# Performance work log

Measured on AMD Instinct MI355X. Metric: run time of the kernel, lower is better.

The kernel has to match this reference:

```python
import jax, jax.numpy as jnp
import numpy as np

B, T, C, H, W = 16, 128, 32, 16, 16
NUM_FEAT = 16
D = C * H * W            # conv1d in-channels (kernel size 1 => linear)
G = NUM_FEAT * H * W     # G3 out-channels


def setup_inputs() -> dict:
    key = jax.random.key(0)
    ks = jax.random.split(key, 8)
    s1 = 1.0 / np.sqrt(D)
    return {
        "input1": jax.random.normal(ks[0], (B, T, C, H, W), jnp.float32),
        "input2": jax.random.normal(ks[1], (B, T, C, H, W), jnp.float32),
        "w1": jax.random.uniform(ks[2], (NUM_FEAT, D), jnp.float32, -s1, s1),
        "b1": jax.random.uniform(ks[3], (NUM_FEAT,), jnp.float32, -s1, s1),
        "w2": jax.random.uniform(ks[4], (NUM_FEAT, D), jnp.float32, -s1, s1),
        "b2": jax.random.uniform(ks[5], (NUM_FEAT,), jnp.float32, -s1, s1),
        "w3": jax.random.uniform(ks[6], (G, D), jnp.float32, -s1, s1),
        "b3": jax.random.uniform(ks[7], (G,), jnp.float32, -s1, s1),
    }


def reference(input1, input2, w1, b1, w2, b2, w3, b3):
    b, t = input1.shape[:2]
    x1 = input1.reshape(b, t, D)  # [B,T,D]
    x2 = input2.reshape(b, t, D)
    # Conv1d(kernel=1) projections (channels-first conv == per-frame linear)
    q = jnp.einsum('btd,fd->btf', x1, w1) + b1          # [B,T,F]
    k = jnp.einsum('bsd,fd->bsf', x2, w2) + b2          # [B,S,F]
    scores = jnp.einsum('btf,bsf->bts', q, k)            # [B,T,T]
    attn = jax.nn.softmax(scores, axis=1)                # softmax over dim=1 (rows)
    v = jnp.einsum('bsd,gd->bsg', x1, w3) + b3           # [B,T,G]
    out = jnp.einsum('bts,bsg->btg', attn, v)            # [B,T,G]
    return out.reshape(b, t, NUM_FEAT, H, W)
```

## Files before the change

### kernel.cpp

```cpp
#include <hip/hip_runtime.h>
#include <cstdint>
#include <cstddef>

#define Bn 16
#define Tn 128
#define Dn 8192
#define Fn 16
#define Gn 4096
#define MT (Bn*Tn)

typedef __attribute__((ext_vector_type(8))) short short8;
typedef __attribute__((ext_vector_type(4))) float f32x4;

__device__ inline short f2bf(float f) {
    union { float f; uint32_t u; } c; c.f = f;
    uint32_t u = c.u;
    uint32_t r = (u + 0x7FFFu + ((u >> 16) & 1u)) >> 16;
    return (short)(r & 0xFFFFu);
}

__device__ inline short8 cvt8(float4 a, float4 b) {
    short8 v;
    v[0] = f2bf(a.x); v[1] = f2bf(a.y); v[2] = f2bf(a.z); v[3] = f2bf(a.w);
    v[4] = f2bf(b.x); v[5] = f2bf(b.y); v[6] = f2bf(b.z); v[7] = f2bf(b.w);
    return v;
}

#define N8_X1 (MT * Dn / 8)
#define N8_W3 ((size_t)Gn * Dn / 8)

__global__ __launch_bounds__(256) void cvt2_kernel(
    const float* __restrict__ x1, const float* __restrict__ w3,
    short* __restrict__ x1b, short* __restrict__ w3b)
{
    const size_t total = N8_X1 + N8_W3;
    size_t i = (size_t)blockIdx.x * 256 + threadIdx.x;
    const size_t stride = (size_t)gridDim.x * 256;
    for (; i < total; i += stride) {
        if (i < N8_X1) {
            const float4* s = ((const float4*)x1) + i * 2;
            ((short8*)x1b)[i] = cvt8(s[0], s[1]);
        } else {
            const size_t j = i - N8_X1;
            const float4* s = ((const float4*)w3) + j * 2;
            ((short8*)w3b)[j] = cvt8(s[0], s[1]);
        }
    }
}

__global__ __launch_bounds__(256) void qk_gemm_kernel(
    const short* __restrict__ x1b, const float* __restrict__ x2,
    const float* __restrict__ w1, const float* __restrict__ w2,
    const float* __restrict__ b1, const float* __restrict__ b2,
    float* __restrict__ q, float* __restrict__ k)
{
    __shared__ float red[4][16][16];
    const int tid = threadIdx.x;
    const int tile = blockIdx.x >> 1;
    const int isK  = blockIdx.x & 1;
    const int m0 = tile * 16;
    const int wave = tid >> 6, lane = tid & 63;
    const int quad = lane >> 4, r = lane & 15;
    const int kbase = wave * (Dn / 4);

    f32x4 acc = {};

    if (!isK) {
        const short* ap = x1b + (size_t)(m0 + r) * Dn + kbase + quad * 8;
        const float* bp = w1 + (size_t)r * Dn + kbase + quad * 8;
        #pragma unroll 4
        for (int it = 0; it < 64; ++it) {
            short8 af = *(const short8*)(ap + it * 32);
            const float4* b4 = (const float4*)(bp + it * 32);
            short8 bf = cvt8(b4[0], b4[1]);
            acc = __builtin_amdgcn_mfma_f32_16x16x32_bf16(af, bf, acc, 0, 0, 0);
        }
    } else {
        const float* apf = x2 + (size_t)(m0 + r) * Dn + kbase + quad * 8;
        const float* bp  = w2 + (size_t)r * Dn + kbase + quad * 8;
        #pragma unroll 4
        for (int it = 0; it < 64; ++it) {
            const float4* a4 = (const float4*)(apf + it * 32);
            short8 af = cvt8(a4[0], a4[1]);
            const float4* b4 = (const float4*)(bp + it * 32);
            short8 bf = cvt8(b4[0], b4[1]);
            acc = __builtin_amdgcn_mfma_f32_16x16x32_bf16(af, bf, acc, 0, 0, 0);
        }
    }

    #pragma unroll
    for (int reg = 0; reg < 4; ++reg)
        red[wave][quad * 4 + reg][r] = acc[reg];
    __syncthreads();

    const int m = tid >> 4, f = tid & 15;
    float s = red[0][m][f] + red[1][m][f] + red[2][m][f] + red[3][m][f];
    s += (isK ? b2 : b1)[f];
    (isK ? k : q)[(m0 + m) * Fn + f] = s;
}

__global__ __launch_bounds__(256) void attn_kernel(
    const float* __restrict__ q, const float* __restrict__ k,
    short* __restrict__ attn16)
{
    __shared__ float qs[Tn * 17];
    const int b = blockIdx.x;
    const int tid = threadIdx.x;
    const int wave = tid >> 6, lane = tid & 63;
    const int s = blockIdx.y * 4 + wave;

    for (int i = tid; i < Tn * Fn; i += 256)
        qs[(i >> 4) * 17 + (i & 15)] = q[b * Tn * Fn + i];
    __syncthreads();

    float kr[16];
    #pragma unroll
    for (int f = 0; f < 16; ++f) kr[f] = k[((size_t)b * Tn + s) * Fn + f];

    const int t0 = lane, t1 = lane + 64;
    float sc0 = 0.f, sc1 = 0.f;
    #pragma unroll
    for (int f = 0; f < 16; ++f) {
        sc0 += qs[t0 * 17 + f] * kr[f];
        sc1 += qs[t1 * 17 + f] * kr[f];
    }
    float m = fmaxf(sc0, sc1);
    #pragma unroll
    for (int off = 32; off > 0; off >>= 1)
        m = fmaxf(m, __shfl_xor(m, off, 64));
    const float e0 = __expf(sc0 - m), e1 = __expf(sc1 - m);
    float ssum = e0 + e1;
    #pragma unroll
    for (int off = 32; off > 0; off >>= 1)
        ssum += __shfl_xor(ssum, off, 64);
    const float inv = 1.f / ssum;

    short* ap = attn16 + (size_t)b * Tn * Tn;
    ap[t0 * Tn + s] = f2bf(e0 * inv);
    ap[t1 * Tn + s] = f2bf(e1 * inv);
}

#define BK 32

__global__ __launch_bounds__(256) void gemm_v_split_kernel(
    const short* __restrict__ A, const short* __restrict__ Bw,
    float* __restrict__ vTf, const int kspan)
{
    __shared__ __attribute__((aligned(16))) short As[128 * BK];
    __shared__ __attribute__((aligned(16))) short Bs[128 * BK];

    const int tid = threadIdx.x;
    const int m0 = blockIdx.y * 128;
    const int n0 = blockIdx.x * 128;
    const int z  = blockIdx.z;
    const int kbase = z * kspan;
    float* outp = vTf + (size_t)z * Gn * MT;
    const int wave = tid >> 6, lane = tid & 63;
    const int wm = (wave >> 1) * 64, wn = (wave & 1) * 64;
    const int quad = lane >> 4, r = lane & 15;

    const int srow = wave * 32 + (lane >> 2);
    const int scol = (lane & 3) * 8;
    const short* gA = A  + (size_t)(m0 + srow) * Dn + kbase + scol;
    const short* gB = Bw + (size_t)(n0 + srow) * Dn + kbase + scol;
    short* lA = &As[srow * BK + scol];
    short* lB = &Bs[srow * BK + scol];

    f32x4 acc[4][4] = {};

    #pragma unroll 1
    for (int k0 = 0; k0 < kspan; k0 += BK) {
        __syncthreads();
        __builtin_amdgcn_global_load_lds(
            (const __attribute__((address_space(1))) void*)(gA + k0),
            (__attribute__((address_space(3))) void*)lA, 16, 0, 0);
        __builtin_amdgcn_global_load_lds(
            (const __attribute__((address_space(1))) void*)(gA + k0 + (size_t)16 * Dn),
            (__attribute__((address_space(3))) void*)(lA + 16 * BK), 16, 0, 0);
        __builtin_amdgcn_global_load_lds(
            (const __attribute__((address_space(1))) void*)(gB + k0),
            (__attribute__((address_space(3))) void*)lB, 16, 0, 0);
        __builtin_amdgcn_global_load_lds(
            (const __attribute__((address_space(1))) void*)(gB + k0 + (size_t)16 * Dn),
            (__attribute__((address_space(3))) void*)(lB + 16 * BK), 16, 0, 0);
        __syncthreads();

        short8 af[4], bf[4];
        #pragma unroll
        for (int i = 0; i < 4; ++i)
            af[i] = *(const short8*)&As[(wm + i * 16 + r) * BK + quad * 8];
        #pragma unroll
        for (int j = 0; j < 4; ++j)
            bf[j] = *(const short8*)&Bs[(wn + j * 16 + r) * BK + quad * 8];

        #pragma unroll
        for (int i = 0; i < 4; ++i)
            #pragma unroll
            for (int j = 0; j < 4; ++j)
                acc[i][j] = __builtin_amdgcn_mfma_f32_16x16x32_bf16(
                    af[i], bf[j], acc[i][j], 0, 0, 0);
    }

    #pragma unroll
    for (int i = 0; i < 4; ++i) {
        #pragma unroll
        for (int reg = 0; reg < 4; ++reg) {
            const int rowg = m0 + wm + i * 16 + quad * 4 + reg;
            #pragma unroll
            for (int j = 0; j < 4; ++j) {
                const int col = n0 + wn + j * 16 + r;
                outp[(size_t)rowg * MT + col] = acc[i][j][reg];
            }
        }
    }
}

__global__ __launch_bounds__(256) void vt_cvt_kernel(
    const float* __restrict__ vTf, const float* __restrict__ bias,
    short* __restrict__ vT, const int nparts)
{
    const size_t N8 = (size_t)Gn * MT / 8;
    size_t i = (size_t)blockIdx.x * 256 + threadIdx.x;
    const size_t stride = (size_t)gridDim.x * 256;
    for (; i < N8; i += stride) {
        const float bv = bias[i >> 8];
        float4 a = {bv, bv, bv, bv}, b = {bv, bv, bv, bv};
        for (int p = 0; p < nparts; ++p) {
            const float4* pp = (const float4*)(vTf + (size_t)p * Gn * MT);
            float4 a1 = pp[i * 2], b1 = pp[i * 2 + 1];
            a.x += a1.x; a.y += a1.y; a.z += a1.z; a.w += a1.w;
            b.x += b1.x; b.y += b1.y; b.z += b1.z; b.w += b1.w;
        }
        ((short8*)vT)[i] = cvt8(a, b);
    }
}

__global__ __launch_bounds__(256) void gemm_v_kernel(
    const short* __restrict__ A, const short* __restrict__ Bw,
    const float* __restrict__ bias, short* __restrict__ vT)
{
    __shared__ __attribute__((aligned(16))) short As[128 * BK];
    __shared__ __attribute__((aligned(16))) short Bs[128 * BK];

    const int tid = threadIdx.x;
    const int m0 = blockIdx.y * 128;
    const int n0 = blockIdx.x * 128;
    const int wave = tid >> 6, lane = tid & 63;
    const int wm = (wave >> 1) * 64, wn = (wave & 1) * 64;
    const int quad = lane >> 4, r = lane & 15;

    const int srow = wave * 32 + (lane >> 2);
    const int scol = (lane & 3) * 8;
    const short* gA = A  + (size_t)(m0 + srow) * Dn + scol;
    const short* gB = Bw + (size_t)(n0 + srow) * Dn + scol;
    short* lA = &As[srow * BK + scol];
    short* lB = &Bs[srow * BK + scol];

    f32x4 acc[4][4] = {};

    #pragma unroll 1
    for (int k0 = 0; k0 < Dn; k0 += BK) {
        __syncthreads();
        __builtin_amdgcn_global_load_lds(
            (const __attribute__((address_space(1))) void*)(gA + k0),
            (__attribute__((address_space(3))) void*)lA, 16, 0, 0);
        __builtin_amdgcn_global_load_lds(
            (const __attribute__((address_space(1))) void*)(gA + k0 + (size_t)16 * Dn),
            (__attribute__((address_space(3))) void*)(lA + 16 * BK), 16, 0, 0);
        __builtin_amdgcn_global_load_lds(
            (const __attribute__((address_space(1))) void*)(gB + k0),
            (__attribute__((address_space(3))) void*)lB, 16, 0, 0);
        __builtin_amdgcn_global_load_lds(
            (const __attribute__((address_space(1))) void*)(gB + k0 + (size_t)16 * Dn),
            (__attribute__((address_space(3))) void*)(lB + 16 * BK), 16, 0, 0);
        __syncthreads();

        short8 af[4], bf[4];
        #pragma unroll
        for (int i = 0; i < 4; ++i)
            af[i] = *(const short8*)&As[(wm + i * 16 + r) * BK + quad * 8];
        #pragma unroll
        for (int j = 0; j < 4; ++j)
            bf[j] = *(const short8*)&Bs[(wn + j * 16 + r) * BK + quad * 8];

        #pragma unroll
        for (int i = 0; i < 4; ++i)
            #pragma unroll
            for (int j = 0; j < 4; ++j)
                acc[i][j] = __builtin_amdgcn_mfma_f32_16x16x32_bf16(
                    af[i], bf[j], acc[i][j], 0, 0, 0);
    }

    #pragma unroll
    for (int i = 0; i < 4; ++i) {
        #pragma unroll
        for (int reg = 0; reg < 4; ++reg) {
            const int rowg = m0 + wm + i * 16 + quad * 4 + reg;
            const float bv = bias[rowg];
            #pragma unroll
            for (int j = 0; j < 4; ++j) {
                const int col = n0 + wn + j * 16 + r;
                vT[(size_t)rowg * MT + col] = f2bf(acc[i][j][reg] + bv);
            }
        }
    }
}

__global__ __launch_bounds__(256) void out_gemm_kernel(
    const short* __restrict__ attn16, const short* __restrict__ vT,
    float* __restrict__ out)
{
    __shared__ __attribute__((aligned(16))) short As[128 * BK];
    __shared__ __attribute__((aligned(16))) short Bs[64 * BK];

    const int tid = threadIdx.x;
    const int b  = blockIdx.y;
    const int n0 = blockIdx.x * 64;
    const int wave = tid >> 6, lane = tid & 63;
    const int wm = (wave >> 1) * 64, wn = (wave & 1) * 32;
    const int quad = lane >> 4, r = lane & 15;

    const int srowA = wave * 32 + (lane >> 2);
    const int srowB = wave * 16 + (lane >> 2);
    const int scol = (lane & 3) * 8;
    const short* gA = attn16 + (size_t)b * Tn * Tn + srowA * Tn + scol;
    const short* gB = vT + (size_t)(n0 + srowB) * MT + b * Tn + scol;
    short* lA = &As[srowA * BK + scol];
    short* lB = &Bs[srowB * BK + scol];

    f32x4 acc[4][2] = {};

    #pragma unroll 1
    for (int k0 = 0; k0 < Tn; k0 += BK) {
        __syncthreads();
        __builtin_amdgcn_global_load_lds(
            (const __attribute__((address_space(1))) void*)(gA + k0),
            (__attribute__((address_space(3))) void*)lA, 16, 0, 0);
        __builtin_amdgcn_global_load_lds(
            (const __attribute__((address_space(1))) void*)(gA + k0 + 16 * Tn),
            (__attribute__((address_space(3))) void*)(lA + 16 * BK), 16, 0, 0);
        __builtin_amdgcn_global_load_lds(
            (const __attribute__((address_space(1))) void*)(gB + k0),
            (__attribute__((address_space(3))) void*)lB, 16, 0, 0);
        __syncthreads();

        short8 af[4], bf[2];
        #pragma unroll
        for (int i = 0; i < 4; ++i)
            af[i] = *(const short8*)&As[(wm + i * 16 + r) * BK + quad * 8];
        #pragma unroll
        for (int j = 0; j < 2; ++j)
            bf[j] = *(const short8*)&Bs[(wn + j * 16 + r) * BK + quad * 8];

        #pragma unroll
        for (int i = 0; i < 4; ++i)
            #pragma unroll
            for (int j = 0; j < 2; ++j)
                acc[i][j] = __builtin_amdgcn_mfma_f32_16x16x32_bf16(
                    af[i], bf[j], acc[i][j], 0, 0, 0);
    }

    #pragma unroll
    for (int j = 0; j < 2; ++j) {
        const int col = n0 + wn + j * 16 + r;
        #pragma unroll
        for (int i = 0; i < 4; ++i) {
            #pragma unroll
            for (int reg = 0; reg < 4; ++reg) {
                const int rowt = wm + i * 16 + quad * 4 + reg;
                out[((size_t)(b * Tn + rowt)) * Gn + col] = acc[i][j][reg];
            }
        }
    }
}

extern "C" void kernel_launch(void* const* d_in, const int* in_sizes, int n_in,
                              void* d_out, int out_size, void* d_ws, size_t ws_size,
                              hipStream_t stream)
{
    const float* x1 = (const float*)d_in[0];
    const float* x2 = (const float*)d_in[1];
    const float* w1 = (const float*)d_in[2];
    const float* b1 = (const float*)d_in[3];
    const float* w2 = (const float*)d_in[4];
    const float* b2 = (const float*)d_in[5];
    const float* w3 = (const float*)d_in[6];
    const float* b3 = (const float*)d_in[7];
    float* out = (float*)d_out;

    float* q      = (float*)d_ws;
    float* k      = q + MT * Fn;
    short* attn16 = (short*)(k + MT * Fn);
    short* vT     = attn16 + (size_t)Bn * Tn * Tn;
    short* x1b    = vT + (size_t)Gn * MT;
    short* w3b    = x1b + (size_t)MT * Dn;
    float* vTf    = (float*)(w3b + (size_t)Gn * Dn);

    const size_t base_need =
        (size_t)MT * Fn * 4 * 2 +
        (size_t)Bn * Tn * Tn * 2 +
        (size_t)Gn * MT * 2 +
        (size_t)MT * Dn * 2 +
        (size_t)Gn * Dn * 2;
    const size_t psize = (size_t)Gn * MT * 4;

    int ksplit = 0;
    if (ws_size >= base_need + 4 * psize)      ksplit = 4;
    else if (ws_size >= base_need + 2 * psize) ksplit = 2;

    cvt2_kernel<<<4096, 256, 0, stream>>>(x1, w3, x1b, w3b);
    qk_gemm_kernel<<<256, 256, 0, stream>>>(x1b, x2, w1, w2, b1, b2, q, k);
    attn_kernel<<<dim3(Bn, Tn / 4), 256, 0, stream>>>(q, k, attn16);

    if (ksplit) {
        gemm_v_split_kernel<<<dim3(MT / 128, Gn / 128, ksplit), 256, 0, stream>>>(
            w3b, x1b, vTf, Dn / ksplit);
        vt_cvt_kernel<<<2048, 256, 0, stream>>>(vTf, b3, vT, ksplit);
    } else {
        gemm_v_kernel<<<dim3(MT / 128, Gn / 128), 256, 0, stream>>>(w3b, x1b, b3, vT);
    }

    out_gemm_kernel<<<dim3(Gn / 64, Bn), 256, 0, stream>>>(attn16, vT, out);
}
```

Measured before the change: 548.9 us.

## Split QK projection over K, widen V GEMM K-tile, cap V split at two

The QK projection GEMM is split four ways along the reduction dimension. Each slice writes partial q/k sums, and the attention kernel adds the partials and the biases when it loads them. This raises the QK kernel from 256 blocks to 1024 to fill more compute units. The V GEMM now stages a 64-wide K tile per LDS load, halving the number of barrier-separated iterations, and its split-K factor is capped at 2 instead of 4, which cuts the fp32 partial traffic and the reduction work. The costs are extra partial-sum memory, a slightly longer attention prologue, and fewer V GEMM blocks.

```diff
diff --git a/kernel.cpp b/kernel.cpp
--- a/kernel.cpp
+++ b/kernel.cpp
@@ -8,6 +8,8 @@
 #define Fn 16
 #define Gn 4096
 #define MT (Bn*Tn)
+
+#define QKP 4
 
 typedef __attribute__((ext_vector_type(8))) short short8;
 typedef __attribute__((ext_vector_type(4))) float f32x4;
@@ -51,17 +53,17 @@
 __global__ __launch_bounds__(256) void qk_gemm_kernel(
     const short* __restrict__ x1b, const float* __restrict__ x2,
     const float* __restrict__ w1, const float* __restrict__ w2,
-    const float* __restrict__ b1, const float* __restrict__ b2,
-    float* __restrict__ q, float* __restrict__ k)
+    float* __restrict__ qp, float* __restrict__ kp)
 {
     __shared__ float red[4][16][16];
     const int tid = threadIdx.x;
     const int tile = blockIdx.x >> 1;
     const int isK  = blockIdx.x & 1;
+    const int kq   = blockIdx.y;
     const int m0 = tile * 16;
     const int wave = tid >> 6, lane = tid & 63;
     const int quad = lane >> 4, r = lane & 15;
-    const int kbase = wave * (Dn / 4);
+    const int kbase = kq * (Dn / QKP) + wave * (Dn / QKP / 4);
 
     f32x4 acc = {};
 
@@ -69,7 +71,7 @@
         const short* ap = x1b + (size_t)(m0 + r) * Dn + kbase + quad * 8;
         const float* bp = w1 + (size_t)r * Dn + kbase + quad * 8;
         #pragma unroll 4
-        for (int it = 0; it < 64; ++it) {
+        for (int it = 0; it < 16; ++it) {
             short8 af = *(const short8*)(ap + it * 32);
             const float4* b4 = (const float4*)(bp + it * 32);
             short8 bf = cvt8(b4[0], b4[1]);
@@ -79,7 +81,7 @@
         const float* apf = x2 + (size_t)(m0 + r) * Dn + kbase + quad * 8;
         const float* bp  = w2 + (size_t)r * Dn + kbase + quad * 8;
         #pragma unroll 4
-        for (int it = 0; it < 64; ++it) {
+        for (int it = 0; it < 16; ++it) {
             const float4* a4 = (const float4*)(apf + it * 32);
             short8 af = cvt8(a4[0], a4[1]);
             const float4* b4 = (const float4*)(bp + it * 32);
@@ -95,12 +97,13 @@
 
     const int m = tid >> 4, f = tid & 15;
     float s = red[0][m][f] + red[1][m][f] + red[2][m][f] + red[3][m][f];
-    s += (isK ? b2 : b1)[f];
-    (isK ? k : q)[(m0 + m) * Fn + f] = s;
+    float* dst = isK ? kp : qp;
+    dst[((size_t)kq * MT + m0 + m) * Fn + f] = s;
 }
 
 __global__ __launch_bounds__(256) void attn_kernel(
-    const float* __restrict__ q, const float* __restrict__ k,
+    const float* __restrict__ qp, const float* __restrict__ kp,
+    const float* __restrict__ b1, const float* __restrict__ b2,
     short* __restrict__ attn16)
 {
     __shared__ float qs[Tn * 17];
@@ -109,13 +112,24 @@
     const int wave = tid >> 6, lane = tid & 63;
     const int s = blockIdx.y * 4 + wave;
 
-    for (int i = tid; i < Tn * Fn; i += 256)
-        qs[(i >> 4) * 17 + (i & 15)] = q[b * Tn * Fn + i];
+    for (int i = tid; i < Tn * Fn; i += 256) {
+        float v = b1[i & 15];
+        #pragma unroll
+        for (int p = 0; p < QKP; ++p)
+            v += qp[(size_t)p * MT * Fn + b * Tn * Fn + i];
+        qs[(i >> 4) * 17 + (i & 15)] = v;
+    }
     __syncthreads();
 
     float kr[16];
     #pragma unroll
-    for (int f = 0; f < 16; ++f) kr[f] = k[((size_t)b * Tn + s) * Fn + f];
+    for (int f = 0; f < 16; ++f) {
+        float v = b2[f];
+        #pragma unroll
+        for (int p = 0; p < QKP; ++p)
+            v += kp[((size_t)p * MT + b * Tn + s) * Fn + f];
+        kr[f] = v;
+    }
 
     const int t0 = lane, t1 = lane + 64;
     float sc0 = 0.f, sc1 = 0.f;
@@ -141,13 +155,14 @@
 }
 
 #define BK 32
+#define BKG 64
 
 __global__ __launch_bounds__(256) void gemm_v_split_kernel(
     const short* __restrict__ A, const short* __restrict__ Bw,
     float* __restrict__ vTf, const int kspan)
 {
-    __shared__ __attribute__((aligned(16))) short As[128 * BK];
-    __shared__ __attribute__((aligned(16))) short Bs[128 * BK];
+    __shared__ __attribute__((aligned(16))) short As[128 * BKG];
+    __shared__ __attribute__((aligned(16))) short Bs[128 * BKG];
 
     const int tid = threadIdx.x;
     const int m0 = blockIdx.y * 128;
@@ -159,46 +174,46 @@
     const int wm = (wave >> 1) * 64, wn = (wave & 1) * 64;
     const int quad = lane >> 4, r = lane & 15;
 
-    const int srow = wave * 32 + (lane >> 2);
-    const int scol = (lane & 3) * 8;
+    const int srow = tid >> 3;
+    const int scol = (tid & 7) * 8;
     const short* gA = A  + (size_t)(m0 + srow) * Dn + kbase + scol;
     const short* gB = Bw + (size_t)(n0 + srow) * Dn + kbase + scol;
-    short* lA = &As[srow * BK + scol];
-    short* lB = &Bs[srow * BK + scol];
+    short* lA = &As[srow * BKG + scol];
+    short* lB = &Bs[srow * BKG + scol];
 
     f32x4 acc[4][4] = {};
 
     #pragma unroll 1
-    for (int k0 = 0; k0 < kspan; k0 += BK) {
-        __syncthreads();
-        __builtin_amdgcn_global_load_lds(
-            (const __attribute__((address_space(1))) void*)(gA + k0),
-            (__attribute__((address_space(3))) void*)lA, 16, 0, 0);
-        __builtin_amdgcn_global_load_lds(
-            (const __attribute__((address_space(1))) void*)(gA + k0 + (size_t)16 * Dn),
-            (__attribute__((address_space(3))) void*)(lA + 16 * BK), 16, 0, 0);
-        __builtin_amdgcn_global_load_lds(
-            (const __attribute__((address_space(1))) void*)(gB + k0),
-            (__attribute__((address_space(3))) void*)lB, 16, 0, 0);
-        __builtin_amdgcn_global_load_lds(
-            (const __attribute__((address_space(1))) void*)(gB + k0 + (size_t)16 * Dn),
-            (__attribute__((address_space(3))) void*)(lB + 16 * BK), 16, 0, 0);
-        __syncthreads();
-
-        short8 af[4], bf[4];
-        #pragma unroll
-        for (int i = 0; i < 4; ++i)
-            af[i] = *(const short8*)&As[(wm + i * 16 + r) * BK + quad * 8];
-        #pragma unroll
-        for (int j = 0; j < 4; ++j)
-            bf[j] = *(const short8*)&Bs[(wn + j * 16 + r) * BK + quad * 8];
-
-        #pragma unroll
-        for (int i = 0; i < 4; ++i)
+    for (int k0 = 0; k0 < kspan; k0 += BKG) {
+        __syncthreads();
+        #pragma unroll
+        for (int t = 0; t < 4; ++t) {
+            __builtin_amdgcn_global_load_lds(
+                (const __attribute__((address_space(1))) void*)(gA + k0 + (size_t)(t * 32) * Dn),
+                (__attribute__((address_space(3))) void*)(lA + t * 32 * BKG), 16, 0, 0);
+            __builtin_amdgcn_global_load_lds(
+                (const __attribute__((address_space(1))) void*)(gB + k0 + (size_t)(t * 32) * Dn),
+                (__attribute__((address_space(3))) void*)(lB + t * 32 * BKG), 16, 0, 0);
+        }
+        __syncthreads();
+
+        #pragma unroll
+        for (int half = 0; half < 2; ++half) {
+            short8 af[4], bf[4];
+            #pragma unroll
+            for (int i = 0; i < 4; ++i)
+                af[i] = *(const short8*)&As[(wm + i * 16 + r) * BKG + half * 32 + quad * 8];
             #pragma unroll
             for (int j = 0; j < 4; ++j)
-                acc[i][j] = __builtin_amdgcn_mfma_f32_16x16x32_bf16(
-                    af[i], bf[j], acc[i][j], 0, 0, 0);
+                bf[j] = *(const short8*)&Bs[(wn + j * 16 + r) * BKG + half * 32 + quad * 8];
+
+            #pragma unroll
+            for (int i = 0; i < 4; ++i)
+                #pragma unroll
+                for (int j = 0; j < 4; ++j)
+                    acc[i][j] = __builtin_amdgcn_mfma_f32_16x16x32_bf16(
+                        af[i], bf[j], acc[i][j], 0, 0, 0);
+        }
     }
 
     #pragma unroll
@@ -388,29 +403,27 @@
     const float* b3 = (const float*)d_in[7];
     float* out = (float*)d_out;
 
-    float* q      = (float*)d_ws;
-    float* k      = q + MT * Fn;
-    short* attn16 = (short*)(k + MT * Fn);
+    float* qp     = (float*)d_ws;
+    float* kp     = qp + (size_t)QKP * MT * Fn;
+    short* attn16 = (short*)(kp + (size_t)QKP * MT * Fn);
     short* vT     = attn16 + (size_t)Bn * Tn * Tn;
     short* x1b    = vT + (size_t)Gn * MT;
     short* w3b    = x1b + (size_t)MT * Dn;
     float* vTf    = (float*)(w3b + (size_t)Gn * Dn);
 
     const size_t base_need =
-        (size_t)MT * Fn * 4 * 2 +
+        (size_t)QKP * MT * Fn * 4 * 2 +
         (size_t)Bn * Tn * Tn * 2 +
         (size_t)Gn * MT * 2 +
         (size_t)MT * Dn * 2 +
         (size_t)Gn * Dn * 2;
     const size_t psize = (size_t)Gn * MT * 4;
 
-    int ksplit = 0;
-    if (ws_size >= base_need + 4 * psize)      ksplit = 4;
-    else if (ws_size >= base_need + 2 * psize) ksplit = 2;
+    const int ksplit = (ws_size >= base_need + 2 * psize) ? 2 : 0;
 
     cvt2_kernel<<<4096, 256, 0, stream>>>(x1, w3, x1b, w3b);
-    qk_gemm_kernel<<<256, 256, 0, stream>>>(x1b, x2, w1, w2, b1, b2, q, k);
-    attn_kernel<<<dim3(Bn, Tn / 4), 256, 0, stream>>>(q, k, attn16);
+    qk_gemm_kernel<<<dim3(256, QKP), 256, 0, stream>>>(x1b, x2, w1, w2, qp, kp);
+    attn_kernel<<<dim3(Bn, Tn / 4), 256, 0, stream>>>(qp, kp, b1, b2, attn16);
 
     if (ksplit) {
         gemm_v_split_kernel<<<dim3(MT / 128, Gn / 128, ksplit), 256, 0, stream>>>(
```

Result: slower. 562.9 us (+2.6%).
